# Kernel tuning notes

Hardware: AMD Instinct MI355X
Metric: run time of the kernel (lower is better)

Reference implementation:

```python
import jax, jax.numpy as jnp
import numpy as np

THRESHOLD = 0.5
CONNECT_EPS = 0.1


def setup_inputs() -> dict:
    key = jax.random.key(0)
    ks = jax.random.split(key, 8)
    B, N, F = 4, 512, 128
    H = jax.random.normal(ks[0], (B, N, F), dtype=jnp.float32)
    A = jax.random.uniform(ks[1], (B, N, N), dtype=jnp.float32)
    s2f, sf = 1.0 / np.sqrt(2 * F), 1.0 / np.sqrt(F)
    dW1 = jax.random.normal(ks[2], (2 * F, F), dtype=jnp.float32) * s2f
    db1 = jnp.zeros((F,), dtype=jnp.float32)
    dW2 = jax.random.normal(ks[3], (F, 1), dtype=jnp.float32) * sf
    db2 = jnp.zeros((1,), dtype=jnp.float32)
    rW1 = jax.random.normal(ks[4], (2 * F + 1, F), dtype=jnp.float32) * s2f
    rb1 = jnp.zeros((F,), dtype=jnp.float32)
    rW2 = jax.random.normal(ks[5], (F, F), dtype=jnp.float32) * sf
    rb2 = jnp.zeros((F,), dtype=jnp.float32)
    return {"H": H, "A": A, "dW1": dW1, "db1": db1, "dW2": dW2, "db2": db2,
            "rW1": rW1, "rb1": rb1, "rW2": rW2, "rb2": rb2}


def reference(H, A, dW1, db1, dW2, db2, rW1, rb1, rW2, rb2):
    B, N, F = H.shape
    # Detector on pairs [H_i ; H_j]: split the first linear so we never build [B,N,N,2F].
    Hi = jnp.einsum('bnf,fh->bnh', H, dW1[:F])           # [B,N,F]
    Hj = jnp.einsum('bnf,fh->bnh', H, dW1[F:])           # [B,N,F]
    h = jax.nn.elu(Hi[:, :, None, :] + Hj[:, None, :, :] + db1)  # [B,N,N,F]
    scores = jax.nn.sigmoid(jnp.einsum('bijh,ho->bijo', h, dW2)[..., 0] + db2[0])  # [B,N,N]
    connected = A > CONNECT_EPS
    contradictions = jnp.where(connected, scores, 0.0)
    max_contra = contradictions.max(axis=-1)             # [B,N]
    contra_mask = max_contra > THRESHOLD                 # [B,N] bool
    # Neighbor mean over A > 0 (strict zero, matching torch.where(A[b,n] > 0))
    nbr = (A > 0).astype(H.dtype)                        # [B,N,N]
    deg = nbr.sum(axis=-1)                               # [B,N]
    neighbor_feat = jnp.einsum('bij,bjf->bif', nbr, H) / jnp.maximum(deg, 1.0)[..., None]
    concat = jnp.concatenate([H, neighbor_feat, max_contra[..., None]], axis=-1)  # [B,N,2F+1]
    res = jax.nn.elu(jnp.einsum('bnf,fh->bnh', concat, rW1) + rb1)
    res = jnp.einsum('bnh,ho->bno', res, rW2) + rb2       # [B,N,F]
    update = contra_mask & (deg > 0)
    H_resolved = jnp.where(update[..., None], res, H)
    return H_resolved, contra_mask
```

## Files before the change

kernel.cpp:

```cpp
#include <hip/hip_runtime.h>
#include <cmath>

#define B_ 4
#define N_ 512
#define F_ 128
#define BN_ (B_*N_)
#define NG_ (BN_/4)

__device__ __forceinline__ float elu_f(float x) {
    return fmaxf(x, __expf(fminf(x, 0.f)) - 1.f);
}

__global__ __launch_bounds__(512, 4) void k_pre(
    const float* __restrict__ H, const float* __restrict__ dW1,
    const float* __restrict__ db1,
    float* __restrict__ Hi, float* __restrict__ EHi, float* __restrict__ HjT,
    float* __restrict__ csp) {
    __shared__ float sH[4][F_];
    __shared__ float sPA[3][4][F_], sPB[3][4][F_];
    const int t = threadIdx.x;
    const int f = t & 127;
    const int kq = t >> 7;
    if (blockIdx.x < NG_) {
        const int row0 = blockIdx.x * 4;
        const int b  = row0 >> 9;
        const int n0 = row0 & 511;
        sH[kq][f] = H[(size_t)(row0 + kq) * F_ + f];
        __syncthreads();
        float accA[4] = {0.f,0.f,0.f,0.f}, accB[4] = {0.f,0.f,0.f,0.f};
        const int k0 = kq * 32;
        #pragma unroll 4
        for (int k = k0; k < k0 + 32; ++k) {
            const float wa = dW1[(size_t)k * F_ + f];
            const float wb = dW1[(size_t)(F_ + k) * F_ + f];
            #pragma unroll
            for (int r = 0; r < 4; ++r) {
                accA[r] = fmaf(sH[r][k], wa, accA[r]);
                accB[r] = fmaf(sH[r][k], wb, accB[r]);
            }
        }
        if (kq > 0) {
            #pragma unroll
            for (int r = 0; r < 4; ++r) {
                sPA[kq - 1][r][f] = accA[r];
                sPB[kq - 1][r][f] = accB[r];
            }
        }
        __syncthreads();
        if (kq == 0) {
            const float bias = db1[f];
            float bsum[4];
            #pragma unroll
            for (int r = 0; r < 4; ++r) {
                const float av = accA[r] + sPA[0][r][f] + sPA[1][r][f]
                               + sPA[2][r][f] + bias;
                Hi [(size_t)(row0 + r) * F_ + f] = av;
                EHi[(size_t)(row0 + r) * F_ + f] = __expf(av);
                bsum[r] = accB[r] + sPB[0][r][f] + sPB[1][r][f] + sPB[2][r][f];
            }
            float4 hv;
            hv.x = bsum[0]; hv.y = bsum[1]; hv.z = bsum[2]; hv.w = bsum[3];
            *reinterpret_cast<float4*>(HjT + ((size_t)b * F_ + f) * N_ + n0) = hv;
        }
    } else {
        const int bx = blockIdx.x - NG_;
        const int b  = bx >> 3;
        const int e  = bx & 7;
        float s = 0.f;
        const float* hp = H + ((size_t)b * N_ + e * 64 + kq * 16) * F_ + f;
        #pragma unroll 4
        for (int jj = 0; jj < 16; ++jj) s += hp[(size_t)jj * F_];
        sH[kq][f] = s;
        __syncthreads();
        if (kq == 0)
            csp[((size_t)b * 8 + e) * F_ + f] =
                sH[0][f] + sH[1][f] + sH[2][f] + sH[3][f];
    }
}

#define SCORE_F(HJ4, CP) {                                                    \
    const float ejx = __expf((HJ4).x), ejy = __expf((HJ4).y),                 \
                ejz = __expf((HJ4).z), ejw = __expf((HJ4).w);                 \
    const float wv_ = wq.CP;                                                  \
    acc0.x = fmaf(__builtin_amdgcn_fmed3f(h0.CP + (HJ4).x, fmaf(e0.CP, ejx, -1.f), 0.f), wv_, acc0.x); \
    acc0.y = fmaf(__builtin_amdgcn_fmed3f(h0.CP + (HJ4).y, fmaf(e0.CP, ejy, -1.f), 0.f), wv_, acc0.y); \
    acc0.z = fmaf(__builtin_amdgcn_fmed3f(h0.CP + (HJ4).z, fmaf(e0.CP, ejz, -1.f), 0.f), wv_, acc0.z); \
    acc0.w = fmaf(__builtin_amdgcn_fmed3f(h0.CP + (HJ4).w, fmaf(e0.CP, ejw, -1.f), 0.f), wv_, acc0.w); \
    acc1.x = fmaf(__builtin_amdgcn_fmed3f(h1.CP + (HJ4).x, fmaf(e1.CP, ejx, -1.f), 0.f), wv_, acc1.x); \
    acc1.y = fmaf(__builtin_amdgcn_fmed3f(h1.CP + (HJ4).y, fmaf(e1.CP, ejy, -1.f), 0.f), wv_, acc1.y); \
    acc1.z = fmaf(__builtin_amdgcn_fmed3f(h1.CP + (HJ4).z, fmaf(e1.CP, ejz, -1.f), 0.f), wv_, acc1.z); \
    acc1.w = fmaf(__builtin_amdgcn_fmed3f(h1.CP + (HJ4).w, fmaf(e1.CP, ejw, -1.f), 0.f), wv_, acc1.w); \
    acc2.x = fmaf(__builtin_amdgcn_fmed3f(h2.CP + (HJ4).x, fmaf(e2.CP, ejx, -1.f), 0.f), wv_, acc2.x); \
    acc2.y = fmaf(__builtin_amdgcn_fmed3f(h2.CP + (HJ4).y, fmaf(e2.CP, ejy, -1.f), 0.f), wv_, acc2.y); \
    acc2.z = fmaf(__builtin_amdgcn_fmed3f(h2.CP + (HJ4).z, fmaf(e2.CP, ejz, -1.f), 0.f), wv_, acc2.z); \
    acc2.w = fmaf(__builtin_amdgcn_fmed3f(h2.CP + (HJ4).w, fmaf(e2.CP, ejw, -1.f), 0.f), wv_, acc2.w); \
    acc3.x = fmaf(__builtin_amdgcn_fmed3f(h3.CP + (HJ4).x, fmaf(e3.CP, ejx, -1.f), 0.f), wv_, acc3.x); \
    acc3.y = fmaf(__builtin_amdgcn_fmed3f(h3.CP + (HJ4).y, fmaf(e3.CP, ejy, -1.f), 0.f), wv_, acc3.y); \
    acc3.z = fmaf(__builtin_amdgcn_fmed3f(h3.CP + (HJ4).z, fmaf(e3.CP, ejz, -1.f), 0.f), wv_, acc3.z); \
    acc3.w = fmaf(__builtin_amdgcn_fmed3f(h3.CP + (HJ4).w, fmaf(e3.CP, ejw, -1.f), 0.f), wv_, acc3.w); }

#define LOADQ_P(P, B0, B1, B2, B3)                                            \
    B0 = *reinterpret_cast<const float4*>((P) + (size_t)0 * N_);              \
    B1 = *reinterpret_cast<const float4*>((P) + (size_t)1 * N_);              \
    B2 = *reinterpret_cast<const float4*>((P) + (size_t)2 * N_);              \
    B3 = *reinterpret_cast<const float4*>((P) + (size_t)3 * N_);

#define COMPQ_DYN(QE, B0, B1, B2, B3) {                                       \
    const int q_ = kq * 8 + (QE);                                             \
    const float4 h0 = sU[q_][0], h1 = sU[q_][1], h2 = sU[q_][2], h3 = sU[q_][3]; \
    const float4 e0 = sU[q_][4], e1 = sU[q_][5], e2 = sU[q_][6], e3 = sU[q_][7]; \
    const float4 wq = sU[q_][8];                                              \
    SCORE_F(B0, x) SCORE_F(B1, y) SCORE_F(B2, z) SCORE_F(B3, w) }

__global__ __launch_bounds__(512) void k_main(
    const float* __restrict__ Hi, const float* __restrict__ EHi,
    const float* __restrict__ HjT, const float* __restrict__ A,
    const float* __restrict__ dW2, const float* __restrict__ db2,
    const float* __restrict__ H, const float* __restrict__ csp,
    const float* __restrict__ rW1, const float* __restrict__ rb1,
    const float* __restrict__ rW2, const float* __restrict__ rb2,
    float* __restrict__ out, float* __restrict__ maskout) {
    __shared__ float4 sU[32][9];
    __shared__ float  sBig[4 * 4 * N_];
    __shared__ float  red_mx[8][4];
    __shared__ int    red_cnt[8][4];
    __shared__ unsigned long long sZb[8][4];
    __shared__ float  sMC[4], sDegF[4];
    const int t = threadIdx.x;
    const int lane = t & 63;
    const int w = t >> 6;
    const int u  = t & 127;
    const int kq = t >> 7;
    const int f  = t & 127;
    const int bi0 = blockIdx.x * 4;
    const int b = bi0 >> 9;

    if (t < 288) {
        const int q  = t / 9;
        const int sl = t - q * 9;
        const float* src = (sl < 4) ? (Hi  + (size_t)(bi0 + sl)     * F_ + 4 * q)
                         : (sl < 8) ? (EHi + (size_t)(bi0 + sl - 4) * F_ + 4 * q)
                                    : (dW2 + 4 * q);
        sU[q][sl] = *reinterpret_cast<const float4*>(src);
    }
    float a_r[4];
    #pragma unroll
    for (int r = 0; r < 4; ++r) a_r[r] = A[(size_t)(bi0 + r) * N_ + t];

    const float* __restrict__ hjq = HjT + (size_t)b * F_ * N_
                                  + (size_t)(kq * 32) * N_ + 4 * u;
    float4 hA0, hA1, hA2, hA3, hB0, hB1, hB2, hB3;
    LOADQ_P(hjq, hA0, hA1, hA2, hA3)
    __syncthreads();

    float4 acc0 = {0.f,0.f,0.f,0.f}, acc1 = {0.f,0.f,0.f,0.f};
    float4 acc2 = {0.f,0.f,0.f,0.f}, acc3 = {0.f,0.f,0.f,0.f};

    #pragma unroll 1
    for (int q = 0; q < 8; q += 2) {
        const float* pB = hjq + (size_t)(q + 1) * 4 * N_;
        LOADQ_P(pB, hB0, hB1, hB2, hB3)
        COMPQ_DYN(q, hA0, hA1, hA2, hA3)
        if (q + 2 < 8) {
            const float* pA = hjq + (size_t)(q + 2) * 4 * N_;
            LOADQ_P(pA, hA0, hA1, hA2, hA3)
        }
        COMPQ_DYN(q + 1, hB0, hB1, hB2, hB3)
    }

    *reinterpret_cast<float4*>(&sBig[(kq * 4 + 0) * N_ + 4 * u]) = acc0;
    *reinterpret_cast<float4*>(&sBig[(kq * 4 + 1) * N_ + 4 * u]) = acc1;
    *reinterpret_cast<float4*>(&sBig[(kq * 4 + 2) * N_ + 4 * u]) = acc2;
    *reinterpret_cast<float4*>(&sBig[(kq * 4 + 3) * N_ + 4 * u]) = acc3;
    __syncthreads();

    #pragma unroll
    for (int r = 0; r < 4; ++r) {
        const float a = a_r[r];
        const float sum = sBig[(0 * 4 + r) * N_ + t] + sBig[(1 * 4 + r) * N_ + t]
                        + sBig[(2 * 4 + r) * N_ + t] + sBig[(3 * 4 + r) * N_ + t];
        float mx = (a > 0.1f) ? sum : -INFINITY;
        #pragma unroll
        for (int off = 1; off < 64; off <<= 1)
            mx = fmaxf(mx, __shfl_xor(mx, off));
        const unsigned long long pos = __ballot(a > 0.f);
        const unsigned long long zb  = __ballot(a <= 0.f);
        if (lane == 0) {
            red_mx[w][r]  = mx;
            red_cnt[w][r] = (int)__popcll(pos);
            sZb[w][r]     = zb;
        }
    }
    __syncthreads();
    if (t < 4) {
        float m = -INFINITY; int c = 0;
        #pragma unroll
        for (int ww = 0; ww < 8; ++ww) {
            m = fmaxf(m, red_mx[ww][t]);
            c += red_cnt[ww][t];
        }
        const float mc = (m > -INFINITY)
                       ? 1.f / (1.f + __expf(-(m + db2[0]))) : 0.f;
        sMC[t]   = mc;
        sDegF[t] = (float)c;
        maskout[bi0 + t] = (mc > 0.5f) ? 1.f : 0.f;
    }
    __syncthreads();

    float* sC  = sBig;
    float* sP  = sBig + 1040;
    float* sL1 = sBig + 2576;

    {
        const int row = bi0 + kq;
        sC[kq * 260 + f] = H[(size_t)row * F_ + f];
        float cs = 0.f;
        #pragma unroll
        for (int e = 0; e < 8; ++e)
            cs += csp[((size_t)b * 8 + e) * F_ + f];
        #pragma unroll
        for (int wv = 0; wv < 8; ++wv) {
            unsigned long long zb = sZb[wv][kq];
            while (zb) {
                const int j = __ffsll(zb) - 1;
                zb &= zb - 1;
                cs -= H[((size_t)b * N_ + wv * 64 + j) * F_ + f];
            }
        }
        sC[kq * 260 + F_ + f] = cs / fmaxf(sDegF[kq], 1.f);
    }
    __syncthreads();

    float macc[4];
    {
        const float bias = rb1[f];
        #pragma unroll
        for (int r = 0; r < 4; ++r) macc[r] = (kq == 0) ? bias : 0.f;
    }
    const int k0 = kq * 64;
    #pragma unroll 4
    for (int kk = 0; kk < 64; kk += 4) {
        const int k = k0 + kk;
        const float4 c0 = *reinterpret_cast<const float4*>(&sC[0 * 260 + k]);
        const float4 c1 = *reinterpret_cast<const float4*>(&sC[1 * 260 + k]);
        const float4 c2 = *reinterpret_cast<const float4*>(&sC[2 * 260 + k]);
        const float4 c3 = *reinterpret_cast<const float4*>(&sC[3 * 260 + k]);
        const float w0 = rW1[(size_t)(k + 0) * F_ + f];
        const float w1 = rW1[(size_t)(k + 1) * F_ + f];
        const float w2 = rW1[(size_t)(k + 2) * F_ + f];
        const float w3 = rW1[(size_t)(k + 3) * F_ + f];
        macc[0] = fmaf(c0.x, w0, macc[0]); macc[1] = fmaf(c1.x, w0, macc[1]);
        macc[2] = fmaf(c2.x, w0, macc[2]); macc[3] = fmaf(c3.x, w0, macc[3]);
        macc[0] = fmaf(c0.y, w1, macc[0]); macc[1] = fmaf(c1.y, w1, macc[1]);
        macc[2] = fmaf(c2.y, w1, macc[2]); macc[3] = fmaf(c3.y, w1, macc[3]);
        macc[0] = fmaf(c0.z, w2, macc[0]); macc[1] = fmaf(c1.z, w2, macc[1]);
        macc[2] = fmaf(c2.z, w2, macc[2]); macc[3] = fmaf(c3.z, w2, macc[3]);
        macc[0] = fmaf(c0.w, w3, macc[0]); macc[1] = fmaf(c1.w, w3, macc[1]);
        macc[2] = fmaf(c2.w, w3, macc[2]); macc[3] = fmaf(c3.w, w3, macc[3]);
    }
    if (kq == 3) {
        const float w256 = rW1[(size_t)256 * F_ + f];
        #pragma unroll
        for (int r = 0; r < 4; ++r) macc[r] = fmaf(sMC[r], w256, macc[r]);
    }
    if (kq > 0) {
        #pragma unroll
        for (int r = 0; r < 4; ++r) sP[((kq - 1) * 4 + r) * F_ + f] = macc[r];
    }
    __syncthreads();
    if (kq == 0) {
        #pragma unroll
        for (int r = 0; r < 4; ++r)
            sL1[r * F_ + f] = elu_f(macc[r] + sP[(0 * 4 + r) * F_ + f]
                                   + sP[(1 * 4 + r) * F_ + f]
                                   + sP[(2 * 4 + r) * F_ + f]);
    }
    __syncthreads();

    float macc2[4];
    {
        const float bias2 = rb2[f];
        #pragma unroll
        for (int r = 0; r < 4; ++r) macc2[r] = (kq == 0) ? bias2 : 0.f;
    }
    const int m0k = kq * 32;
    #pragma unroll 4
    for (int kk = 0; kk < 32; kk += 4) {
        const int k = m0k + kk;
        const float4 l0 = *reinterpret_cast<const float4*>(&sL1[0 * F_ + k]);
        const float4 l1 = *reinterpret_cast<const float4*>(&sL1[1 * F_ + k]);
        const float4 l2 = *reinterpret_cast<const float4*>(&sL1[2 * F_ + k]);
        const float4 l3 = *reinterpret_cast<const float4*>(&sL1[3 * F_ + k]);
        const float w0 = rW2[(size_t)(k + 0) * F_ + f];
        const float w1 = rW2[(size_t)(k + 1) * F_ + f];
        const float w2 = rW2[(size_t)(k + 2) * F_ + f];
        const float w3 = rW2[(size_t)(k + 3) * F_ + f];
        macc2[0] = fmaf(l0.x, w0, macc2[0]); macc2[1] = fmaf(l1.x, w0, macc2[1]);
        macc2[2] = fmaf(l2.x, w0, macc2[2]); macc2[3] = fmaf(l3.x, w0, macc2[3]);
        macc2[0] = fmaf(l0.y, w1, macc2[0]); macc2[1] = fmaf(l1.y, w1, macc2[1]);
        macc2[2] = fmaf(l2.y, w1, macc2[2]); macc2[3] = fmaf(l3.y, w1, macc2[3]);
        macc2[0] = fmaf(l0.z, w2, macc2[0]); macc2[1] = fmaf(l1.z, w2, macc2[1]);
        macc2[2] = fmaf(l2.z, w2, macc2[2]); macc2[3] = fmaf(l3.z, w2, macc2[3]);
        macc2[0] = fmaf(l0.w, w3, macc2[0]); macc2[1] = fmaf(l1.w, w3, macc2[1]);
        macc2[2] = fmaf(l2.w, w3, macc2[2]); macc2[3] = fmaf(l3.w, w3, macc2[3]);
    }
    if (kq > 0) {
        #pragma unroll
        for (int r = 0; r < 4; ++r) sP[((kq - 1) * 4 + r) * F_ + f] = macc2[r];
    }
    __syncthreads();
    if (kq == 0) {
        #pragma unroll
        for (int r = 0; r < 4; ++r) {
            const int row = bi0 + r;
            const float res = macc2[r] + sP[(0 * 4 + r) * F_ + f]
                            + sP[(1 * 4 + r) * F_ + f]
                            + sP[(2 * 4 + r) * F_ + f];
            const bool upd = (sMC[r] > 0.5f) && (sDegF[r] > 0.f);
            out[(size_t)row * F_ + f] = upd ? res : sC[r * 260 + f];
        }
    }
}

extern "C" void kernel_launch(void* const* d_in, const int* in_sizes, int n_in,
                              void* d_out, int out_size, void* d_ws, size_t ws_size,
                              hipStream_t stream) {
    const float* H   = (const float*)d_in[0];
    const float* A   = (const float*)d_in[1];
    const float* dW1 = (const float*)d_in[2];
    const float* db1 = (const float*)d_in[3];
    const float* dW2 = (const float*)d_in[4];
    const float* db2 = (const float*)d_in[5];
    const float* rW1 = (const float*)d_in[6];
    const float* rb1 = (const float*)d_in[7];
    const float* rW2 = (const float*)d_in[8];
    const float* rb2 = (const float*)d_in[9];

    float* ws  = (float*)d_ws;
    float* Hi  = ws;
    float* EHi = Hi  + BN_ * F_;
    float* HjT = EHi + BN_ * F_;
    float* csp = HjT + BN_ * F_;

    float* out      = (float*)d_out;
    float* mask_out = out + BN_ * F_;

    k_pre <<<NG_ + 32, 512, 0, stream>>>(H, dW1, db1, Hi, EHi, HjT, csp);
    k_main<<<NG_, 512, 0, stream>>>(Hi, EHi, HjT, A, dW2, db2,
                                    H, csp, rW1, rb1, rW2, rb2,
                                    out, mask_out);
}
```

Measured before the change: 42.40 us.

## Process two rows per block in k_main to double grid and occupancy

```diff
diff --git a/kernel.cpp b/kernel.cpp
--- a/kernel.cpp
+++ b/kernel.cpp
@@ -6,6 +6,7 @@
 #define F_ 128
 #define BN_ (B_*N_)
 #define NG_ (BN_/4)
+#define NG2_ (BN_/2)
 
 __device__ __forceinline__ float elu_f(float x) {
     return fmaxf(x, __expf(fminf(x, 0.f)) - 1.f);
@@ -78,7 +79,7 @@
     }
 }
 
-#define SCORE_F(HJ4, CP) {                                                    \
+#define SCORE_F2(HJ4, CP) {                                                   \
     const float ejx = __expf((HJ4).x), ejy = __expf((HJ4).y),                 \
                 ejz = __expf((HJ4).z), ejw = __expf((HJ4).w);                 \
     const float wv_ = wq.CP;                                                  \
@@ -89,15 +90,7 @@
     acc1.x = fmaf(__builtin_amdgcn_fmed3f(h1.CP + (HJ4).x, fmaf(e1.CP, ejx, -1.f), 0.f), wv_, acc1.x); \
     acc1.y = fmaf(__builtin_amdgcn_fmed3f(h1.CP + (HJ4).y, fmaf(e1.CP, ejy, -1.f), 0.f), wv_, acc1.y); \
     acc1.z = fmaf(__builtin_amdgcn_fmed3f(h1.CP + (HJ4).z, fmaf(e1.CP, ejz, -1.f), 0.f), wv_, acc1.z); \
-    acc1.w = fmaf(__builtin_amdgcn_fmed3f(h1.CP + (HJ4).w, fmaf(e1.CP, ejw, -1.f), 0.f), wv_, acc1.w); \
-    acc2.x = fmaf(__builtin_amdgcn_fmed3f(h2.CP + (HJ4).x, fmaf(e2.CP, ejx, -1.f), 0.f), wv_, acc2.x); \
-    acc2.y = fmaf(__builtin_amdgcn_fmed3f(h2.CP + (HJ4).y, fmaf(e2.CP, ejy, -1.f), 0.f), wv_, acc2.y); \
-    acc2.z = fmaf(__builtin_amdgcn_fmed3f(h2.CP + (HJ4).z, fmaf(e2.CP, ejz, -1.f), 0.f), wv_, acc2.z); \
-    acc2.w = fmaf(__builtin_amdgcn_fmed3f(h2.CP + (HJ4).w, fmaf(e2.CP, ejw, -1.f), 0.f), wv_, acc2.w); \
-    acc3.x = fmaf(__builtin_amdgcn_fmed3f(h3.CP + (HJ4).x, fmaf(e3.CP, ejx, -1.f), 0.f), wv_, acc3.x); \
-    acc3.y = fmaf(__builtin_amdgcn_fmed3f(h3.CP + (HJ4).y, fmaf(e3.CP, ejy, -1.f), 0.f), wv_, acc3.y); \
-    acc3.z = fmaf(__builtin_amdgcn_fmed3f(h3.CP + (HJ4).z, fmaf(e3.CP, ejz, -1.f), 0.f), wv_, acc3.z); \
-    acc3.w = fmaf(__builtin_amdgcn_fmed3f(h3.CP + (HJ4).w, fmaf(e3.CP, ejw, -1.f), 0.f), wv_, acc3.w); }
+    acc1.w = fmaf(__builtin_amdgcn_fmed3f(h1.CP + (HJ4).w, fmaf(e1.CP, ejw, -1.f), 0.f), wv_, acc1.w); }
 
 #define LOADQ_P(P, B0, B1, B2, B3)                                            \
     B0 = *reinterpret_cast<const float4*>((P) + (size_t)0 * N_);              \
@@ -105,14 +98,14 @@
     B2 = *reinterpret_cast<const float4*>((P) + (size_t)2 * N_);              \
     B3 = *reinterpret_cast<const float4*>((P) + (size_t)3 * N_);
 
-#define COMPQ_DYN(QE, B0, B1, B2, B3) {                                       \
+#define COMPQ2(QE, B0, B1, B2, B3) {                                          \
     const int q_ = kq * 8 + (QE);                                             \
-    const float4 h0 = sU[q_][0], h1 = sU[q_][1], h2 = sU[q_][2], h3 = sU[q_][3]; \
-    const float4 e0 = sU[q_][4], e1 = sU[q_][5], e2 = sU[q_][6], e3 = sU[q_][7]; \
-    const float4 wq = sU[q_][8];                                              \
-    SCORE_F(B0, x) SCORE_F(B1, y) SCORE_F(B2, z) SCORE_F(B3, w) }
-
-__global__ __launch_bounds__(512) void k_main(
+    const float4 h0 = sU[q_][0], h1 = sU[q_][1];                              \
+    const float4 e0 = sU[q_][2], e1 = sU[q_][3];                              \
+    const float4 wq = sU[q_][4];                                              \
+    SCORE_F2(B0, x) SCORE_F2(B1, y) SCORE_F2(B2, z) SCORE_F2(B3, w) }
+
+__global__ __launch_bounds__(512, 8) void k_main(
     const float* __restrict__ Hi, const float* __restrict__ EHi,
     const float* __restrict__ HjT, const float* __restrict__ A,
     const float* __restrict__ dW2, const float* __restrict__ db2,
@@ -120,65 +113,56 @@
     const float* __restrict__ rW1, const float* __restrict__ rb1,
     const float* __restrict__ rW2, const float* __restrict__ rb2,
     float* __restrict__ out, float* __restrict__ maskout) {
-    __shared__ float4 sU[32][9];
-    __shared__ float  sBig[4 * 4 * N_];
-    __shared__ float  red_mx[8][4];
-    __shared__ int    red_cnt[8][4];
-    __shared__ unsigned long long sZb[8][4];
-    __shared__ float  sMC[4], sDegF[4];
+    __shared__ float4 sU[32][5];
+    __shared__ float  sBig[4 * 2 * N_];
+    __shared__ float  red_mx[8][2];
+    __shared__ int    red_cnt[8][2];
+    __shared__ unsigned long long sZb[8][2];
+    __shared__ float  sMC[2], sDegF[2];
     const int t = threadIdx.x;
     const int lane = t & 63;
     const int w = t >> 6;
     const int u  = t & 127;
     const int kq = t >> 7;
     const int f  = t & 127;
-    const int bi0 = blockIdx.x * 4;
+    const int bi0 = blockIdx.x * 2;
     const int b = bi0 >> 9;
 
-    if (t < 288) {
-        const int q  = t / 9;
-        const int sl = t - q * 9;
-        const float* src = (sl < 4) ? (Hi  + (size_t)(bi0 + sl)     * F_ + 4 * q)
-                         : (sl < 8) ? (EHi + (size_t)(bi0 + sl - 4) * F_ + 4 * q)
+    if (t < 160) {
+        const int q  = t / 5;
+        const int sl = t - q * 5;
+        const float* src = (sl < 2) ? (Hi  + (size_t)(bi0 + sl)     * F_ + 4 * q)
+                         : (sl < 4) ? (EHi + (size_t)(bi0 + sl - 2) * F_ + 4 * q)
                                     : (dW2 + 4 * q);
         sU[q][sl] = *reinterpret_cast<const float4*>(src);
     }
-    float a_r[4];
+    float a_r[2];
     #pragma unroll
-    for (int r = 0; r < 4; ++r) a_r[r] = A[(size_t)(bi0 + r) * N_ + t];
+    for (int r = 0; r < 2; ++r) a_r[r] = A[(size_t)(bi0 + r) * N_ + t];
 
     const float* __restrict__ hjq = HjT + (size_t)b * F_ * N_
                                   + (size_t)(kq * 32) * N_ + 4 * u;
-    float4 hA0, hA1, hA2, hA3, hB0, hB1, hB2, hB3;
-    LOADQ_P(hjq, hA0, hA1, hA2, hA3)
     __syncthreads();
 
     float4 acc0 = {0.f,0.f,0.f,0.f}, acc1 = {0.f,0.f,0.f,0.f};
-    float4 acc2 = {0.f,0.f,0.f,0.f}, acc3 = {0.f,0.f,0.f,0.f};
 
     #pragma unroll 1
-    for (int q = 0; q < 8; q += 2) {
-        const float* pB = hjq + (size_t)(q + 1) * 4 * N_;
-        LOADQ_P(pB, hB0, hB1, hB2, hB3)
-        COMPQ_DYN(q, hA0, hA1, hA2, hA3)
-        if (q + 2 < 8) {
-            const float* pA = hjq + (size_t)(q + 2) * 4 * N_;
-            LOADQ_P(pA, hA0, hA1, hA2, hA3)
-        }
-        COMPQ_DYN(q + 1, hB0, hB1, hB2, hB3)
-    }
-
-    *reinterpret_cast<float4*>(&sBig[(kq * 4 + 0) * N_ + 4 * u]) = acc0;
-    *reinterpret_cast<float4*>(&sBig[(kq * 4 + 1) * N_ + 4 * u]) = acc1;
-    *reinterpret_cast<float4*>(&sBig[(kq * 4 + 2) * N_ + 4 * u]) = acc2;
-    *reinterpret_cast<float4*>(&sBig[(kq * 4 + 3) * N_ + 4 * u]) = acc3;
+    for (int q = 0; q < 8; ++q) {
+        const float* p = hjq + (size_t)q * 4 * N_;
+        float4 hA0, hA1, hA2, hA3;
+        LOADQ_P(p, hA0, hA1, hA2, hA3)
+        COMPQ2(q, hA0, hA1, hA2, hA3)
+    }
+
+    *reinterpret_cast<float4*>(&sBig[(kq * 2 + 0) * N_ + 4 * u]) = acc0;
+    *reinterpret_cast<float4*>(&sBig[(kq * 2 + 1) * N_ + 4 * u]) = acc1;
     __syncthreads();
 
     #pragma unroll
-    for (int r = 0; r < 4; ++r) {
+    for (int r = 0; r < 2; ++r) {
         const float a = a_r[r];
-        const float sum = sBig[(0 * 4 + r) * N_ + t] + sBig[(1 * 4 + r) * N_ + t]
-                        + sBig[(2 * 4 + r) * N_ + t] + sBig[(3 * 4 + r) * N_ + t];
+        const float sum = sBig[(0 * 2 + r) * N_ + t] + sBig[(1 * 2 + r) * N_ + t]
+                        + sBig[(2 * 2 + r) * N_ + t] + sBig[(3 * 2 + r) * N_ + t];
         float mx = (a > 0.1f) ? sum : -INFINITY;
         #pragma unroll
         for (int off = 1; off < 64; off <<= 1)
@@ -192,7 +176,7 @@
         }
     }
     __syncthreads();
-    if (t < 4) {
+    if (t < 2) {
         float m = -INFINITY; int c = 0;
         #pragma unroll
         for (int ww = 0; ww < 8; ++ww) {
@@ -208,10 +192,10 @@
     __syncthreads();
 
     float* sC  = sBig;
-    float* sP  = sBig + 1040;
-    float* sL1 = sBig + 2576;
-
-    {
+    float* sP  = sBig + 520;
+    float* sL1 = sBig + 1288;
+
+    if (kq < 2) {
         const int row = bi0 + kq;
         sC[kq * 260 + f] = H[(size_t)row * F_ + f];
         float cs = 0.f;
@@ -231,11 +215,11 @@
     }
     __syncthreads();
 
-    float macc[4];
+    float macc[2];
     {
         const float bias = rb1[f];
         #pragma unroll
-        for (int r = 0; r < 4; ++r) macc[r] = (kq == 0) ? bias : 0.f;
+        for (int r = 0; r < 2; ++r) macc[r] = (kq == 0) ? bias : 0.f;
     }
     const int k0 = kq * 64;
     #pragma unroll 4
@@ -243,45 +227,39 @@
         const int k = k0 + kk;
         const float4 c0 = *reinterpret_cast<const float4*>(&sC[0 * 260 + k]);
         const float4 c1 = *reinterpret_cast<const float4*>(&sC[1 * 260 + k]);
-        const float4 c2 = *reinterpret_cast<const float4*>(&sC[2 * 260 + k]);
-        const float4 c3 = *reinterpret_cast<const float4*>(&sC[3 * 260 + k]);
         const float w0 = rW1[(size_t)(k + 0) * F_ + f];
         const float w1 = rW1[(size_t)(k + 1) * F_ + f];
         const float w2 = rW1[(size_t)(k + 2) * F_ + f];
         const float w3 = rW1[(size_t)(k + 3) * F_ + f];
         macc[0] = fmaf(c0.x, w0, macc[0]); macc[1] = fmaf(c1.x, w0, macc[1]);
-        macc[2] = fmaf(c2.x, w0, macc[2]); macc[3] = fmaf(c3.x, w0, macc[3]);
         macc[0] = fmaf(c0.y, w1, macc[0]); macc[1] = fmaf(c1.y, w1, macc[1]);
-        macc[2] = fmaf(c2.y, w1, macc[2]); macc[3] = fmaf(c3.y, w1, macc[3]);
         macc[0] = fmaf(c0.z, w2, macc[0]); macc[1] = fmaf(c1.z, w2, macc[1]);
-        macc[2] = fmaf(c2.z, w2, macc[2]); macc[3] = fmaf(c3.z, w2, macc[3]);
         macc[0] = fmaf(c0.w, w3, macc[0]); macc[1] = fmaf(c1.w, w3, macc[1]);
-        macc[2] = fmaf(c2.w, w3, macc[2]); macc[3] = fmaf(c3.w, w3, macc[3]);
     }
     if (kq == 3) {
         const float w256 = rW1[(size_t)256 * F_ + f];
         #pragma unroll
-        for (int r = 0; r < 4; ++r) macc[r] = fmaf(sMC[r], w256, macc[r]);
+        for (int r = 0; r < 2; ++r) macc[r] = fmaf(sMC[r], w256, macc[r]);
     }
     if (kq > 0) {
         #pragma unroll
-        for (int r = 0; r < 4; ++r) sP[((kq - 1) * 4 + r) * F_ + f] = macc[r];
+        for (int r = 0; r < 2; ++r) sP[((kq - 1) * 2 + r) * F_ + f] = macc[r];
     }
     __syncthreads();
     if (kq == 0) {
         #pragma unroll
-        for (int r = 0; r < 4; ++r)
-            sL1[r * F_ + f] = elu_f(macc[r] + sP[(0 * 4 + r) * F_ + f]
-                                   + sP[(1 * 4 + r) * F_ + f]
-                                   + sP[(2 * 4 + r) * F_ + f]);
-    }
-    __syncthreads();
-
-    float macc2[4];
+        for (int r = 0; r < 2; ++r)
+            sL1[r * F_ + f] = elu_f(macc[r] + sP[(0 * 2 + r) * F_ + f]
+                                   + sP[(1 * 2 + r) * F_ + f]
+                                   + sP[(2 * 2 + r) * F_ + f]);
+    }
+    __syncthreads();
+
+    float macc2[2];
     {
         const float bias2 = rb2[f];
         #pragma unroll
-        for (int r = 0; r < 4; ++r) macc2[r] = (kq == 0) ? bias2 : 0.f;
+        for (int r = 0; r < 2; ++r) macc2[r] = (kq == 0) ? bias2 : 0.f;
     }
     const int m0k = kq * 32;
     #pragma unroll 4
@@ -289,33 +267,27 @@
         const int k = m0k + kk;
         const float4 l0 = *reinterpret_cast<const float4*>(&sL1[0 * F_ + k]);
         const float4 l1 = *reinterpret_cast<const float4*>(&sL1[1 * F_ + k]);
-        const float4 l2 = *reinterpret_cast<const float4*>(&sL1[2 * F_ + k]);
-        const float4 l3 = *reinterpret_cast<const float4*>(&sL1[3 * F_ + k]);
         const float w0 = rW2[(size_t)(k + 0) * F_ + f];
         const float w1 = rW2[(size_t)(k + 1) * F_ + f];
         const float w2 = rW2[(size_t)(k + 2) * F_ + f];
         const float w3 = rW2[(size_t)(k + 3) * F_ + f];
         macc2[0] = fmaf(l0.x, w0, macc2[0]); macc2[1] = fmaf(l1.x, w0, macc2[1]);
-        macc2[2] = fmaf(l2.x, w0, macc2[2]); macc2[3] = fmaf(l3.x, w0, macc2[3]);
         macc2[0] = fmaf(l0.y, w1, macc2[0]); macc2[1] = fmaf(l1.y, w1, macc2[1]);
-        macc2[2] = fmaf(l2.y, w1, macc2[2]); macc2[3] = fmaf(l3.y, w1, macc2[3]);
         macc2[0] = fmaf(l0.z, w2, macc2[0]); macc2[1] = fmaf(l1.z, w2, macc2[1]);
-        macc2[2] = fmaf(l2.z, w2, macc2[2]); macc2[3] = fmaf(l3.z, w2, macc2[3]);
         macc2[0] = fmaf(l0.w, w3, macc2[0]); macc2[1] = fmaf(l1.w, w3, macc2[1]);
-        macc2[2] = fmaf(l2.w, w3, macc2[2]); macc2[3] = fmaf(l3.w, w3, macc2[3]);
     }
     if (kq > 0) {
         #pragma unroll
-        for (int r = 0; r < 4; ++r) sP[((kq - 1) * 4 + r) * F_ + f] = macc2[r];
+        for (int r = 0; r < 2; ++r) sP[((kq - 1) * 2 + r) * F_ + f] = macc2[r];
     }
     __syncthreads();
     if (kq == 0) {
         #pragma unroll
-        for (int r = 0; r < 4; ++r) {
+        for (int r = 0; r < 2; ++r) {
             const int row = bi0 + r;
-            const float res = macc2[r] + sP[(0 * 4 + r) * F_ + f]
-                            + sP[(1 * 4 + r) * F_ + f]
-                            + sP[(2 * 4 + r) * F_ + f];
+            const float res = macc2[r] + sP[(0 * 2 + r) * F_ + f]
+                            + sP[(1 * 2 + r) * F_ + f]
+                            + sP[(2 * 2 + r) * F_ + f];
             const bool upd = (sMC[r] > 0.5f) && (sDegF[r] > 0.f);
             out[(size_t)row * F_ + f] = upd ? res : sC[r * 260 + f];
         }
@@ -346,7 +318,7 @@
     float* mask_out = out + BN_ * F_;
 
     k_pre <<<NG_ + 32, 512, 0, stream>>>(H, dW1, db1, Hi, EHi, HjT, csp);
-    k_main<<<NG_, 512, 0, stream>>>(Hi, EHi, HjT, A, dW2, db2,
-                                    H, csp, rW1, rb1, rW2, rb2,
-                                    out, mask_out);
+    k_main<<<NG2_, 512, 0, stream>>>(Hi, EHi, HjT, A, dW2, db2,
+                                     H, csp, rW1, rb1, rW2, rb2,
+                                     out, mask_out);
 }
```

Result: no change. 43.05 us (+1.5%).
